# Kernel optimization log

Measured on AMD Instinct MI355X. Metric: run time of the kernel, lower is better.

## Reference

```python
import jax, jax.numpy as jnp
import numpy as np

N, E = 50000, 800000          # nodes, edges
IN, H, OUT = 256, 128, 2       # input feat, hidden_channels, out_channels
NEG_SLOPE = 0.2                # GATv2 LeakyReLU slope (PyG default)


def _w(key, fan_in, fan_out):
    return jax.random.normal(key, (fan_in, fan_out), jnp.float32) / np.sqrt(fan_in).astype(np.float32)


def setup_inputs() -> dict:
    key = jax.random.key(0)
    ks = jax.random.split(key, 24)
    inp = {
        "x": jax.random.normal(ks[0], (N, IN), jnp.float32),
        "edge_index": jax.random.randint(ks[1], (2, E), 0, N, jnp.int32),
        # GATv2Conv 0: in=IN -> H
        "c0_Wl": _w(ks[2], IN, H), "c0_Wr": _w(ks[3], IN, H),
        "c0_att": jax.random.normal(ks[4], (H,), jnp.float32) / np.sqrt(H).astype(np.float32),
        "c0_b": jnp.zeros((H,), jnp.float32),
        # GATv2Conv 1: H -> H
        "c1_Wl": _w(ks[5], H, H), "c1_Wr": _w(ks[6], H, H),
        "c1_att": jax.random.normal(ks[7], (H,), jnp.float32) / np.sqrt(H).astype(np.float32),
        "c1_b": jnp.zeros((H,), jnp.float32),
        # final GATv2Conv: H -> OUT
        "cf_Wl": _w(ks[8], H, OUT), "cf_Wr": _w(ks[9], H, OUT),
        "cf_att": jax.random.normal(ks[10], (OUT,), jnp.float32) / np.sqrt(OUT).astype(np.float32),
        "cf_b": jnp.zeros((OUT,), jnp.float32),
        # residual Linears
        "l0_W": _w(ks[11], IN, H), "l0_b": jnp.zeros((H,), jnp.float32),
        "l1_W": _w(ks[12], H, H), "l1_b": jnp.zeros((H,), jnp.float32),
        "lf_W": _w(ks[13], H, OUT), "lf_b": jnp.zeros((OUT,), jnp.float32),
    }
    return inp


def gatv2(x, edge_index, Wl, Wr, att, bias):
    """PyG GATv2Conv, heads=1, add_self_loops=False, share_weights=False."""
    src, dst = edge_index[0], edge_index[1]
    xs = x @ Wl                                   # [N,H] source transform
    xd = x @ Wr                                   # [N,H] target transform
    h = jax.nn.leaky_relu(xs[src] + xd[dst], NEG_SLOPE)   # [E,H]
    e = h @ att                                   # [E] attention logits
    # segment softmax over incoming edges of each destination node
    m = jax.ops.segment_max(e, dst, num_segments=N)
    m = jnp.where(jnp.isfinite(m), m, 0.0)
    p = jnp.exp(e - m[dst])
    s = jax.ops.segment_sum(p, dst, num_segments=N)
    alpha = p / (s[dst] + 1e-16)                  # [E]
    out = jax.ops.segment_sum(alpha[:, None] * xs[src], dst, num_segments=N)
    return out + bias


def reference(x, edge_index, c0_Wl, c0_Wr, c0_att, c0_b, c1_Wl, c1_Wr, c1_att, c1_b,
              cf_Wl, cf_Wr, cf_att, cf_b, l0_W, l0_b, l1_W, l1_b, lf_W, lf_b):
    # layer 0 + residual linear, then ReLU
    h = gatv2(x, edge_index, c0_Wl, c0_Wr, c0_att, c0_b) + (jax.nn.relu(x) @ l0_W + l0_b)
    h = jax.nn.relu(h)
    # layer 1 -> embeddings
    emb = gatv2(h, edge_index, c1_Wl, c1_Wr, c1_att, c1_b) + (jax.nn.relu(h) @ l1_W + l1_b)
    # final layer -> logits
    out = gatv2(emb, edge_index, cf_Wl, cf_Wr, cf_att, cf_b) + (jax.nn.relu(emb) @ lf_W + lf_b)
    return (out, emb)
```

## Files before the change

kernel.cpp:

```cpp
#include <hip/hip_runtime.h>
#include <hip/hip_bf16.h>

#define NEG_SLOPE 0.2f

typedef __attribute__((ext_vector_type(8))) _Float16 half8;
typedef __attribute__((ext_vector_type(2))) _Float16 h2v;
typedef __attribute__((ext_vector_type(4))) float f32x4;

__device__ __forceinline__ float toF(float x) { return x; }
__device__ __forceinline__ float toF(__hip_bfloat16 x) { return __bfloat162float(x); }
__device__ __forceinline__ float toF(_Float16 x) { return (float)x; }

__device__ __forceinline__ void stT(float* p, size_t i, float v) { p[i] = v; }
__device__ __forceinline__ void stT(__hip_bfloat16* p, size_t i, float v) {
    p[i] = __float2bfloat16(v);
}
__device__ __forceinline__ void stT(_Float16* p, size_t i, float v) { p[i] = (_Float16)v; }

template <typename T> struct IsBF { static constexpr bool v = false; };
template <> struct IsBF<__hip_bfloat16> { static constexpr bool v = true; };

__device__ __forceinline__ void vwaitn(int n) {
    if (n == 0) asm volatile("s_waitcnt vmcnt(0)" ::: "memory");
    else if (n == 7) asm volatile("s_waitcnt vmcnt(7)" ::: "memory");
    else if (n == 8) asm volatile("s_waitcnt vmcnt(8)" ::: "memory");
    else if (n == 9) asm volatile("s_waitcnt vmcnt(9)" ::: "memory");
    else asm volatile("s_waitcnt vmcnt(10)" ::: "memory");
}

__global__ void k_detect(const unsigned* __restrict__ x, int* __restrict__ flag) {
    unsigned u = x[threadIdx.x];
    int lo_exp = (int)((u >> 7) & 0xFFu);
    int ok = (lo_exp >= 90 && lo_exp <= 141) ? 1 : 0;
    unsigned long long b = __ballot(ok);
    if (threadIdx.x == 0) flag[0] = (__popcll(b) >= 48) ? 1 : 0;
}

__global__ __launch_bounds__(256) void k_cnt(const int* __restrict__ src,
                                             const int* __restrict__ dst, int E,
                                             int* __restrict__ gcnt,
                                             unsigned* __restrict__ bbuf, int cap) {
    __shared__ int hist[64];
    __shared__ int lbase[64];
    __shared__ int gbase[64];
    __shared__ int lfill[64];
    __shared__ unsigned ebuf[4096];
    __shared__ unsigned char bb[4096];
    int t = threadIdx.x;
    int e0 = blockIdx.x * 4096;
    if (t < 64) { hist[t] = 0; lfill[t] = 0; }
    __syncthreads();
    unsigned my[16];
    int mybkt[16];
#pragma unroll
    for (int i = 0; i < 16; ++i) {
        int idx = e0 + i * 256 + t;
        if (idx < E) {
            int d = dst[idx];
            int b = d >> 10;
            mybkt[i] = b;
            my[i] = (unsigned)src[idx] | ((unsigned)(d & 1023) << 16);
            atomicAdd(&hist[b], 1);
        } else {
            mybkt[i] = -1;
        }
    }
    __syncthreads();
    if (t < 64) {
        int h = hist[t];
        int v = h;
#pragma unroll
        for (int o = 1; o < 64; o <<= 1) {
            int u = __shfl_up(v, o, 64);
            if (t >= o) v += u;
        }
        lbase[t] = v - h;
        gbase[t] = (h > 0) ? atomicAdd(&gcnt[t], h) : 0;
    }
    __syncthreads();
#pragma unroll
    for (int i = 0; i < 16; ++i) {
        int b = mybkt[i];
        if (b >= 0) {
            int p = lbase[b] + atomicAdd(&lfill[b], 1);
            ebuf[p] = my[i];
            bb[p] = (unsigned char)b;
        }
    }
    __syncthreads();
    int total = min(4096, E - e0);
    for (int p = t; p < total; p += 256) {
        int b = bb[p];
        int o = gbase[b] + (p - lbase[b]);
        if (o < cap) bbuf[(size_t)b * cap + o] = ebuf[p];
    }
}

__global__ __launch_bounds__(256) void k_bucket_hist(const int* __restrict__ gcnt,
                                                     const unsigned* __restrict__ bbuf, int cap,
                                                     int* __restrict__ rowptr, int n) {
    __shared__ int hist[1024];
    int b = blockIdx.x, t = threadIdx.x;
    for (int i = t; i < 1024; i += 256) hist[i] = 0;
    __syncthreads();
    int cnt = min(gcnt[b], cap);
    const unsigned* p = bbuf + (size_t)b * cap;
    for (int i = t; i < cnt; i += 256) atomicAdd(&hist[p[i] >> 16], 1);
    __syncthreads();
    for (int i = t; i < 1024; i += 256) {
        int d = b * 1024 + i;
        if (d < n) rowptr[d + 1] = hist[i];
    }
}

__global__ __launch_bounds__(256) void k_bplace(const int* __restrict__ gcnt,
                                                const unsigned* __restrict__ bbuf, int cap,
                                                const int* __restrict__ rowptr,
                                                int* __restrict__ csr_src, int n) {
    __shared__ int base[1024];
    __shared__ int fill[1024];
    int b = blockIdx.x, t = threadIdx.x;
    for (int i = t; i < 1024; i += 256) {
        int d = b * 1024 + i;
        base[i] = (d < n) ? rowptr[d] : 0;
        fill[i] = 0;
    }
    __syncthreads();
    int cnt = min(gcnt[b], cap);
    const unsigned* p = bbuf + (size_t)b * cap;
    for (int i = t; i < cnt; i += 256) {
        unsigned e = p[i];
        int dl = (int)(e >> 16);
        int pos = base[dl] + atomicAdd(&fill[dl], 1);
        csr_src[pos] = (int)(e & 0xFFFFu);
    }
}

__global__ void k_hist(const int* __restrict__ dst, int E, int* __restrict__ rowptr) {
    int i = blockIdx.x * blockDim.x + threadIdx.x;
    if (i < E) atomicAdd(&rowptr[dst[i] + 1], 1);
}

__global__ void k_scatter(const int* __restrict__ src, const int* __restrict__ dst, int E,
                          const int* __restrict__ rowptr, int* __restrict__ fill,
                          int* __restrict__ csr_src) {
    int i = blockIdx.x * blockDim.x + threadIdx.x;
    if (i < E) {
        int d = dst[i];
        int pos = rowptr[d] + atomicAdd(&fill[d], 1);
        csr_src[pos] = src[i];
    }
}

__global__ __launch_bounds__(256) void k_scan1(int* __restrict__ rowptr,
                                               int* __restrict__ blksum, int n) {
    __shared__ int wsum[4];
    int t = threadIdx.x, lane = t & 63, w = t >> 6;
    int idx = blockIdx.x * 1024 + t * 4;
    int c0 = (idx + 0 < n) ? rowptr[idx + 1] : 0;
    int c1 = (idx + 1 < n) ? rowptr[idx + 2] : 0;
    int c2 = (idx + 2 < n) ? rowptr[idx + 3] : 0;
    int c3 = (idx + 3 < n) ? rowptr[idx + 4] : 0;
    int s1 = c0 + c1, s2 = s1 + c2, s3 = s2 + c3;
    int v = s3;
#pragma unroll
    for (int o = 1; o < 64; o <<= 1) {
        int u = __shfl_up(v, o, 64);
        if (lane >= o) v += u;
    }
    if (lane == 63) wsum[w] = v;
    __syncthreads();
    int woff = 0;
#pragma unroll
    for (int i = 0; i < 3; ++i)
        if (i < w) woff += wsum[i];
    int excl = woff + v - s3;
    if (idx + 0 < n) rowptr[idx + 1] = excl + c0;
    if (idx + 1 < n) rowptr[idx + 2] = excl + s1;
    if (idx + 2 < n) rowptr[idx + 3] = excl + s2;
    if (idx + 3 < n) rowptr[idx + 4] = excl + s3;
    if (t == 255) blksum[blockIdx.x] = woff + v;
}

__global__ void k_scan2(int* __restrict__ blksum, int nblk) {
    int t = threadIdx.x;
    int v = (t < nblk) ? blksum[t] : 0;
#pragma unroll
    for (int o = 1; o < 64; o <<= 1) {
        int u = __shfl_up(v, o, 64);
        if (t >= o) v += u;
    }
    if (t < nblk) blksum[t] = v;
}

__global__ void k_scan3(int* __restrict__ rowptr, const int* __restrict__ blksum, int n) {
    int idx = blockIdx.x * blockDim.x + threadIdx.x;
    if (idx < n) {
        int b = idx >> 10;
        if (b > 0) rowptr[idx + 1] += blksum[b - 1];
    }
}

template <typename WT>
__device__ void packW_body(const WT* W0, const WT* W1, const WT* W2, const WT* b2, int K,
                           _Float16* Bp, float* biasf) {
    int lane = threadIdx.x;
    int ksteps = K >> 5;
    int nb = 3 * ksteps * 8;
    int bid = blockIdx.x;
    if (bid == nb) {
        biasf[lane * 2 + 0] = toF(b2[lane * 2 + 0]);
        biasf[lane * 2 + 1] = toF(b2[lane * 2 + 1]);
        return;
    }
    int ks = bid / 24;
    int rem = bid - ks * 24;
    int o = rem >> 3, ct = rem & 7;
    const WT* W = (o == 0) ? W0 : ((o == 1) ? W1 : W2);
    int c = ct * 16 + (lane & 15);
    int k0 = ks * 32 + (lane >> 4) * 8;
    _Float16* out = Bp + (size_t)bid * 512 + lane * 8;
#pragma unroll
    for (int i = 0; i < 8; ++i) out[i] = (_Float16)toF(W[(size_t)(k0 + i) * 128 + c]);
}

__global__ void k_packW(const int* __restrict__ flag, const void* W0, const void* W1,
                        const void* W2, const void* b2, int K, _Float16* __restrict__ Bp,
                        float* __restrict__ biasf) {
    if (flag[0] == 0)
        packW_body<float>((const float*)W0, (const float*)W1, (const float*)W2,
                          (const float*)b2, K, Bp, biasf);
    else
        packW_body<__hip_bfloat16>((const __hip_bfloat16*)W0, (const __hip_bfloat16*)W1,
                                   (const __hip_bfloat16*)W2, (const __hip_bfloat16*)b2, K,
                                   Bp, biasf);
}

template <typename AT, typename O2T, int KSTEPS>
__device__ void gemm_body(const AT* __restrict__ A, int N,
                          const _Float16* __restrict__ Bp, const float* __restrict__ biasf,
                          _Float16* __restrict__ O0, _Float16* __restrict__ O1,
                          O2T* __restrict__ O2, _Float16 (*sB)[12288]) {
    const int H = 128;
    const int K = KSTEPS * 32;
    int tid = threadIdx.x;
    int wave = tid >> 6, lane = tid & 63;
    int row0 = (blockIdx.x * 4 + wave) * 16;
    int rr = lane & 15, kg = lane >> 4;
    int arow = min(row0 + rr, N - 1);
    constexpr int NR = (sizeof(AT) == 4) ? 2 : 1;

    f32x4 acc[3][8];
#pragma unroll
    for (int o = 0; o < 3; ++o)
#pragma unroll
        for (int ct = 0; ct < 8; ++ct) acc[o][ct] = f32x4{0.f, 0.f, 0.f, 0.f};

    auto stage = [&](int b, int ksv) {
        const char* gsrc = (const char*)(Bp + (size_t)ksv * 12288) + wave * 1024 + lane * 16;
        char* lbase = (char*)(&sB[b][0]) + wave * 1024;
#pragma unroll
        for (int r = 0; r < 6; ++r) {
            __builtin_amdgcn_global_load_lds(
                (const __attribute__((address_space(1))) unsigned*)(gsrc + r * 4096),
                (__attribute__((address_space(3))) unsigned*)(lbase + r * 4096), 16, 0, 0);
        }
    };
    auto loadA = [&](int ksv, uint4* dst) {
        const char* p = (const char*)A + ((size_t)arow * K + ksv * 32 + kg * 8) * sizeof(AT);
        dst[0] = *(const uint4*)p;
        if constexpr (NR == 2) dst[1] = *(const uint4*)(p + 16);
    };
    auto compute = [&](const uint4* raw, const _Float16* sb) {
        half8 a0, a1, r0f, r1f;
        if constexpr (sizeof(AT) == 4) {
            union { uint4 u[2]; float f[8]; } cv;
            cv.u[0] = raw[0]; cv.u[1] = raw[1];
#pragma unroll
            for (int i = 0; i < 8; ++i) {
                float a = cv.f[i];
                _Float16 h = (_Float16)a;
                float lof = a - (float)h;
                _Float16 lo = (_Float16)lof;
                bool pos = a > 0.f;
                a0[i] = h; a1[i] = lo;
                r0f[i] = pos ? h : (_Float16)0.f;
                r1f[i] = pos ? lo : (_Float16)0.f;
            }
        } else if constexpr (IsBF<AT>::v) {
            union { uint4 u4; unsigned u[4]; } cv;
            cv.u4 = raw[0];
#pragma unroll
            for (int q = 0; q < 4; ++q) {
                union { unsigned u; float f; } lo, hi;
                lo.u = cv.u[q] << 16;
                hi.u = cv.u[q] & 0xFFFF0000u;
                a0[2 * q] = (_Float16)lo.f;
                a0[2 * q + 1] = (_Float16)hi.f;
                r0f[2 * q] = (_Float16)fmaxf(lo.f, 0.f);
                r0f[2 * q + 1] = (_Float16)fmaxf(hi.f, 0.f);
            }
        } else {
            union { uint4 u4; half8 h; } cv;
            cv.u4 = raw[0];
            a0 = cv.h;
#pragma unroll
            for (int i = 0; i < 8; ++i)
                r0f[i] = (a0[i] > (_Float16)0.f) ? a0[i] : (_Float16)0.f;
        }
#pragma unroll
        for (int ct = 0; ct < 8; ++ct) {
            half8 w0 = *(const half8*)(sb + (0 * 8 + ct) * 512 + lane * 8);
            half8 w1 = *(const half8*)(sb + (1 * 8 + ct) * 512 + lane * 8);
            half8 w2 = *(const half8*)(sb + (2 * 8 + ct) * 512 + lane * 8);
            acc[0][ct] = __builtin_amdgcn_mfma_f32_16x16x32_f16(a0, w0, acc[0][ct], 0, 0, 0);
            acc[1][ct] = __builtin_amdgcn_mfma_f32_16x16x32_f16(a0, w1, acc[1][ct], 0, 0, 0);
            acc[2][ct] = __builtin_amdgcn_mfma_f32_16x16x32_f16(r0f, w2, acc[2][ct], 0, 0, 0);
            if constexpr (sizeof(AT) == 4) {
                acc[0][ct] = __builtin_amdgcn_mfma_f32_16x16x32_f16(a1, w0, acc[0][ct], 0, 0, 0);
                acc[1][ct] = __builtin_amdgcn_mfma_f32_16x16x32_f16(a1, w1, acc[1][ct], 0, 0, 0);
                acc[2][ct] = __builtin_amdgcn_mfma_f32_16x16x32_f16(r1f, w2, acc[2][ct], 0, 0, 0);
            }
        }
    };

    uint4 rA[3][NR];
    loadA(0, rA[0]);
    loadA(1, rA[1]);
    stage(0, 0);
#pragma unroll
    for (int ks = 0; ks < KSTEPS; ++ks) {
        if (ks + 1 < KSTEPS) {
            stage((ks + 1) & 1, ks + 1);
            asm volatile("" ::: "memory");
        }
        if (ks + 2 < KSTEPS) loadA(ks + 2, rA[(ks + 2) % 3]);
        if (ks == 0 || ks == KSTEPS - 2) vwaitn(NR + 6);
        else if (ks + 2 < KSTEPS) vwaitn(2 * NR + 6);
        else vwaitn(0);
        __builtin_amdgcn_s_barrier();
        compute(rA[ks % 3], &sB[ks & 1][0]);
        __builtin_amdgcn_s_barrier();
    }

    int rb = row0 + kg * 4;
#pragma unroll
    for (int ct = 0; ct < 8; ++ct) {
        int c = ct * 16 + rr;
        float bv = biasf[c];
#pragma unroll
        for (int j = 0; j < 4; ++j) {
            int row = rb + j;
            if (row < N) {
                size_t o = (size_t)row * H + c;
                O0[o] = (_Float16)acc[0][ct][j];
                O1[o] = (_Float16)acc[1][ct][j];
                stT(O2, o, acc[2][ct][j] + bv);
            }
        }
    }
}

template <int LAYER>
__global__ __launch_bounds__(256) void gemm3_u(const int* __restrict__ flag, const void* Aext,
                                               const _Float16* Af16, int N,
                                               const _Float16* __restrict__ Bp,
                                               const float* __restrict__ biasf,
                                               _Float16* __restrict__ O0,
                                               _Float16* __restrict__ O1, _Float16* O2h,
                                               float* O2f, __hip_bfloat16* O2b) {
    __shared__ _Float16 sB[2][12288];
    int f = flag[0];
    if constexpr (LAYER == 0) {
        if (f == 0)
            gemm_body<float, _Float16, 8>((const float*)Aext, N, Bp, biasf, O0, O1, O2h, sB);
        else
            gemm_body<__hip_bfloat16, _Float16, 8>((const __hip_bfloat16*)Aext, N, Bp, biasf,
                                                   O0, O1, O2h, sB);
    } else {
        if (f == 0)
            gemm_body<_Float16, float, 4>(Af16, N, Bp, biasf, O0, O1, O2f, sB);
        else
            gemm_body<_Float16, __hip_bfloat16, 4>(Af16, N, Bp, biasf, O0, O1, O2b, sB);
    }
}

template <typename IOT, typename T, int FINAL>
__device__ void gat_body(const _Float16* __restrict__ xs, const _Float16* __restrict__ xd,
                         const int* __restrict__ rowptr, const int* __restrict__ csr_src,
                         IOT* __restrict__ io, const T* __restrict__ att,
                         const T* __restrict__ gbias, int n, int relu_out,
                         const T* __restrict__ Wl, const T* __restrict__ Wr,
                         const T* __restrict__ Wres, const T* __restrict__ bres,
                         float* __restrict__ xsf, float* __restrict__ xdf,
                         float* __restrict__ resf) {
    int tid = threadIdx.x;
    int l = tid & 15;
    int g = tid >> 4;
    int dst = blockIdx.x * 16 + g;
    if (blockIdx.x * 16 + ((tid >> 6) << 2) >= n) return;
    int dstc = min(dst, n - 1);
    bool act = dst < n;

    union U4H { uint4 u; h2v h[4]; };
    U4H du; du.u = *(const uint4*)(xd + (size_t)dstc * 128 + l * 8);
    h2v ap[4];
#pragma unroll
    for (int c = 0; c < 4; ++c) {
        ap[c][0] = (_Float16)toF(att[l * 8 + 2 * c]);
        ap[c][1] = (_Float16)toF(att[l * 8 + 2 * c + 1]);
    }
    const _Float16 ks = (_Float16)NEG_SLOPE;
    const h2v k02 = {ks, ks};

    int beg = rowptr[dstc];
    int end = act ? rowptr[dstc + 1] : beg;
    float m = -INFINITY, s = 0.f;
    h2v acc[4];
#pragma unroll
    for (int c = 0; c < 4; ++c) acc[c] = h2v{(_Float16)0.f, (_Float16)0.f};

    for (int j = beg; j < end; j += 8) {
        int rem = end - j;
        U4H v[8];
#pragma unroll
        for (int q = 0; q < 8; ++q) {
            int idx = j + ((rem > q) ? q : 0);
            int sq = csr_src[idx];
            v[q].u = *(const uint4*)(xs + (size_t)sq * 128 + l * 8);
        }
        float p[8];
#pragma unroll
        for (int q = 0; q < 8; ++q) p[q] = 0.f;
#pragma unroll
        for (int c = 0; c < 4; ++c) {
#pragma unroll
            for (int q = 0; q < 8; ++q) {
                h2v t = v[q].h[c] + du.h[c];
                t = __builtin_elementwise_max(t, t * k02);
                p[q] = __builtin_amdgcn_fdot2(t, ap[c], p[q], false);
            }
        }
#pragma unroll
        for (int o = 1; o < 16; o <<= 1) {
#pragma unroll
            for (int q = 0; q < 8; ++q) p[q] += __shfl_xor(p[q], o, 16);
        }
#pragma unroll
        for (int q = 1; q < 8; ++q)
            if (rem < q + 1) p[q] = -INFINITY;
        float pm = p[0];
#pragma unroll
        for (int q = 1; q < 8; ++q) pm = fmaxf(pm, p[q]);
        float nm = fmaxf(m, pm);
        float sc = __expf(m - nm);
        float w[8];
        float ws = 0.f;
#pragma unroll
        for (int q = 0; q < 8; ++q) {
            w[q] = __expf(p[q] - nm);
            ws += w[q];
        }
        s = s * sc + ws;
        _Float16 sch = (_Float16)sc;
        h2v scp = {sch, sch};
        h2v wp[8];
#pragma unroll
        for (int q = 0; q < 8; ++q) {
            _Float16 wh = (_Float16)w[q];
            wp[q] = h2v{wh, wh};
        }
#pragma unroll
        for (int c = 0; c < 4; ++c) {
            h2v a = acc[c] * scp;
#pragma unroll
            for (int q = 0; q < 8; ++q) a = a + v[q].h[c] * wp[q];
            acc[c] = a;
        }
        m = nm;
    }

    if (act) {
        float r = 1.f / (s + 1e-16f);
        size_t base = (size_t)dst * 128 + l * 8;
        float ev[8];
#pragma unroll
        for (int c = 0; c < 4; ++c) {
            int f0 = l * 8 + 2 * c;
            float v0 = (float)acc[c][0] * r + toF(gbias[f0]) + toF(io[base + 2 * c]);
            float v1 = (float)acc[c][1] * r + toF(gbias[f0 + 1]) + toF(io[base + 2 * c + 1]);
            if (relu_out) { v0 = fmaxf(v0, 0.f); v1 = fmaxf(v1, 0.f); }
            stT(io, base + 2 * c, v0);
            stT(io, base + 2 * c + 1, v1);
            ev[2 * c] = v0;
            ev[2 * c + 1] = v1;
        }
        if constexpr (FINAL) {
            float d[6] = {0.f, 0.f, 0.f, 0.f, 0.f, 0.f};
#pragma unroll
            for (int f = 0; f < 8; ++f) {
                int fg = (l * 8 + f) * 2;
                float e = ev[f];
                float rp = fmaxf(e, 0.f);
                d[0] += e * toF(Wl[fg]);
                d[1] += e * toF(Wl[fg + 1]);
                d[2] += e * toF(Wr[fg]);
                d[3] += e * toF(Wr[fg + 1]);
                d[4] += rp * toF(Wres[fg]);
                d[5] += rp * toF(Wres[fg + 1]);
            }
#pragma unroll
            for (int i = 0; i < 6; ++i) {
#pragma unroll
                for (int o = 1; o < 16; o <<= 1) d[i] += __shfl_xor(d[i], o, 16);
            }
            if (l == 0) {
                xsf[dst * 2 + 0] = d[0];
                xsf[dst * 2 + 1] = d[1];
                xdf[dst * 2 + 0] = d[2];
                xdf[dst * 2 + 1] = d[3];
                resf[dst * 2 + 0] = d[4] + toF(bres[0]);
                resf[dst * 2 + 1] = d[5] + toF(bres[1]);
            }
        }
    }
}

template <int FINAL>
__global__ __launch_bounds__(256) void gat_u(const int* __restrict__ flag,
                                             const _Float16* __restrict__ xs,
                                             const _Float16* __restrict__ xd,
                                             const int* __restrict__ rowptr,
                                             const int* __restrict__ csr_src, _Float16* io_h,
                                             float* io_f, __hip_bfloat16* io_b, const void* att,
                                             const void* gbias, int n, int relu_out,
                                             const void* Wl, const void* Wr, const void* Wres,
                                             const void* bres, float* xsf, float* xdf,
                                             float* resf) {
    typedef __hip_bfloat16 bf;
    int f = flag[0];
    if constexpr (FINAL == 0) {
        if (f == 0)
            gat_body<_Float16, float, 0>(xs, xd, rowptr, csr_src, io_h, (const float*)att,
                                         (const float*)gbias, n, relu_out, nullptr, nullptr,
                                         nullptr, nullptr, nullptr, nullptr, nullptr);
        else
            gat_body<_Float16, bf, 0>(xs, xd, rowptr, csr_src, io_h, (const bf*)att,
                                      (const bf*)gbias, n, relu_out, nullptr, nullptr, nullptr,
                                      nullptr, nullptr, nullptr, nullptr);
    } else {
        if (f == 0)
            gat_body<float, float, 1>(xs, xd, rowptr, csr_src, io_f, (const float*)att,
                                      (const float*)gbias, n, relu_out, (const float*)Wl,
                                      (const float*)Wr, (const float*)Wres, (const float*)bres,
                                      xsf, xdf, resf);
        else
            gat_body<bf, bf, 1>(xs, xd, rowptr, csr_src, io_b, (const bf*)att, (const bf*)gbias,
                                n, relu_out, (const bf*)Wl, (const bf*)Wr, (const bf*)Wres,
                                (const bf*)bres, xsf, xdf, resf);
    }
}

template <typename T>
__device__ void fe_body(const float* __restrict__ xsf, const float* __restrict__ xdf,
                        const float* __restrict__ resf, const int* __restrict__ rowptr,
                        const int* __restrict__ csr_src, const T* __restrict__ att,
                        const T* __restrict__ gb, T* __restrict__ out, int n) {
    int dst = blockIdx.x * blockDim.x + threadIdx.x;
    if (dst >= n) return;
    float2 dv = ((const float2*)xdf)[dst];
    float a0 = toF(att[0]), a1 = toF(att[1]);
    float m = -INFINITY, s = 0.f, acc0 = 0.f, acc1 = 0.f;
    int beg = rowptr[dst], end = rowptr[dst + 1];
    for (int j = beg; j < end; j += 4) {
        int rem = end - j;
        int i1 = (rem > 1) ? 1 : 0, i2 = (rem > 2) ? 2 : 0, i3 = (rem > 3) ? 3 : 0;
        int s0 = csr_src[j];
        int s1 = csr_src[j + i1];
        int s2 = csr_src[j + i2];
        int s3 = csr_src[j + i3];
        float2 v0 = ((const float2*)xsf)[s0];
        float2 v1 = ((const float2*)xsf)[s1];
        float2 v2 = ((const float2*)xsf)[s2];
        float2 v3 = ((const float2*)xsf)[s3];
        float h0, h1, e0, e1, e2, e3;
        h0 = v0.x + dv.x; h0 = fmaxf(h0, NEG_SLOPE * h0);
        h1 = v0.y + dv.y; h1 = fmaxf(h1, NEG_SLOPE * h1);
        e0 = h0 * a0 + h1 * a1;
        h0 = v1.x + dv.x; h0 = fmaxf(h0, NEG_SLOPE * h0);
        h1 = v1.y + dv.y; h1 = fmaxf(h1, NEG_SLOPE * h1);
        e1 = h0 * a0 + h1 * a1;
        h0 = v2.x + dv.x; h0 = fmaxf(h0, NEG_SLOPE * h0);
        h1 = v2.y + dv.y; h1 = fmaxf(h1, NEG_SLOPE * h1);
        e2 = h0 * a0 + h1 * a1;
        h0 = v3.x + dv.x; h0 = fmaxf(h0, NEG_SLOPE * h0);
        h1 = v3.y + dv.y; h1 = fmaxf(h1, NEG_SLOPE * h1);
        e3 = h0 * a0 + h1 * a1;
        if (rem < 2) e1 = -INFINITY;
        if (rem < 3) e2 = -INFINITY;
        if (rem < 4) e3 = -INFINITY;
        float pm = fmaxf(fmaxf(e0, e1), fmaxf(e2, e3));
        float nm = fmaxf(m, pm);
        float sc = __expf(m - nm);
        float w0 = __expf(e0 - nm), w1 = __expf(e1 - nm);
        float w2 = __expf(e2 - nm), w3 = __expf(e3 - nm);
        s = s * sc + ((w0 + w1) + (w2 + w3));
        acc0 = acc0 * sc + ((w0 * v0.x + w1 * v1.x) + (w2 * v2.x + w3 * v3.x));
        acc1 = acc1 * sc + ((w0 * v0.y + w1 * v1.y) + (w2 * v2.y + w3 * v3.y));
        m = nm;
    }
    float r = 1.f / (s + 1e-16f);
    float2 rv = ((const float2*)resf)[dst];
    stT(out, (size_t)dst * 2 + 0, acc0 * r + toF(gb[0]) + rv.x);
    stT(out, (size_t)dst * 2 + 1, acc1 * r + toF(gb[1]) + rv.y);
}

__global__ void final_edge_u(const int* __restrict__ flag, const float* __restrict__ xsf,
                             const float* __restrict__ xdf, const float* __restrict__ resf,
                             const int* __restrict__ rowptr, const int* __restrict__ csr_src,
                             const void* att, const void* gb, void* out, int n) {
    typedef __hip_bfloat16 bf;
    if (flag[0] == 0)
        fe_body<float>(xsf, xdf, resf, rowptr, csr_src, (const float*)att, (const float*)gb,
                       (float*)out, n);
    else
        fe_body<bf>(xsf, xdf, resf, rowptr, csr_src, (const bf*)att, (const bf*)gb, (bf*)out, n);
}

extern "C" void kernel_launch(void* const* d_in, const int* in_sizes, int n_in,
                              void* d_out, int out_size, void* d_ws, size_t ws_size,
                              hipStream_t stream) {
    typedef __hip_bfloat16 bf;
    typedef _Float16 f16;
    const int IN = 256, H = 128;
    const int N = in_sizes[0] / IN;
    const int E = in_sizes[1] / 2;

    const int* ei = (const int*)d_in[1];

    size_t off = 0;
    auto alloc = [&](size_t bytes) {
        void* p = (char*)d_ws + off;
        off += (bytes + 255) & ~(size_t)255;
        return p;
    };
    f16* xs = (f16*)alloc((size_t)N * H * 2);
    f16* xd = (f16*)alloc((size_t)N * H * 2);
    f16* hb = (f16*)alloc((size_t)N * H * 2);
    int* flag = (int*)alloc(256);
    int* rowptr = (int*)alloc((size_t)(N + 1) * 4);
    int* fill = (int*)alloc((size_t)N * 4);
    int* blksum = (int*)alloc(256 * 4);
    int* csr_src = (int*)alloc((size_t)E * 4);
    float* xsf = (float*)alloc((size_t)N * 2 * 4);
    float* xdf = (float*)alloc((size_t)N * 2 * 4);
    float* resf = (float*)alloc((size_t)N * 2 * 4);
    f16* Bp0 = (f16*)alloc((size_t)3 * 8 * 8 * 512 * 2);
    f16* Bp1 = (f16*)alloc((size_t)3 * 4 * 8 * 512 * 2);
    float* bias0 = (float*)alloc(128 * 4);
    float* bias1 = (float*)alloc(128 * 4);
    const int NB = (N + 1023) / 1024;
    const int CAP = ((2 * (E / (NB > 0 ? NB : 1) + 1) + 255) / 256) * 256;
    int* gcnt = (int*)alloc(64 * 4);
    unsigned* bbuf = (unsigned*)alloc((size_t)NB * CAP * 4);

    const int* e_src = ei;
    const int* e_dst = ei + E;

    k_detect<<<1, 64, 0, stream>>>((const unsigned*)d_in[0], flag);
    const int nblk = (N + 1023) / 1024;
    if (N <= 65536) {
        hipMemsetAsync(rowptr, 0, 4, stream);
        hipMemsetAsync(gcnt, 0, 64 * 4, stream);
        k_cnt<<<(E + 4095) / 4096, 256, 0, stream>>>(e_src, e_dst, E, gcnt, bbuf, CAP);
        k_bucket_hist<<<NB, 256, 0, stream>>>(gcnt, bbuf, CAP, rowptr, N);
        k_scan1<<<nblk, 256, 0, stream>>>(rowptr, blksum, N);
        k_scan2<<<1, 64, 0, stream>>>(blksum, nblk);
        k_scan3<<<(N + 255) / 256, 256, 0, stream>>>(rowptr, blksum, N);
        k_bplace<<<NB, 256, 0, stream>>>(gcnt, bbuf, CAP, rowptr, csr_src, N);
    } else {
        hipMemsetAsync(rowptr, 0, (size_t)(N + 1) * 4, stream);
        hipMemsetAsync(fill, 0, (size_t)N * 4, stream);
        k_hist<<<(E + 255) / 256, 256, 0, stream>>>(e_dst, E, rowptr);
        k_scan1<<<nblk, 256, 0, stream>>>(rowptr, blksum, N);
        k_scan2<<<1, 64, 0, stream>>>(blksum, nblk);
        k_scan3<<<(N + 255) / 256, 256, 0, stream>>>(rowptr, blksum, N);
        k_scatter<<<(E + 255) / 256, 256, 0, stream>>>(e_src, e_dst, E, rowptr, fill, csr_src);
    }

    k_packW<<<3 * 8 * 8 + 1, 64, 0, stream>>>(flag, d_in[2], d_in[3], d_in[14], d_in[15], IN,
                                              Bp0, bias0);
    k_packW<<<3 * 4 * 8 + 1, 64, 0, stream>>>(flag, d_in[6], d_in[7], d_in[16], d_in[17], H,
                                              Bp1, bias1);

    const int g64 = (N + 63) / 64;
    const int eblk16 = (N + 15) / 16;

    float* embF = (float*)d_out + (size_t)N * 2;
    bf* embB = (bf*)d_out + (size_t)N * 2;

    gemm3_u<0><<<g64, 256, 0, stream>>>(flag, d_in[0], nullptr, N, Bp0, bias0, xs, xd, hb,
                                        nullptr, nullptr);
    gat_u<0><<<eblk16, 256, 0, stream>>>(flag, xs, xd, rowptr, csr_src, hb, nullptr, nullptr,
                                         d_in[4], d_in[5], N, 1, nullptr, nullptr, nullptr,
                                         nullptr, nullptr, nullptr, nullptr);

    gemm3_u<1><<<g64, 256, 0, stream>>>(flag, nullptr, hb, N, Bp1, bias1, xs, xd, nullptr,
                                        embF, embB);
    gat_u<1><<<eblk16, 256, 0, stream>>>(flag, xs, xd, rowptr, csr_src, nullptr, embF, embB,
                                         d_in[8], d_in[9], N, 0, d_in[10], d_in[11], d_in[18],
                                         d_in[19], xsf, xdf, resf);

    final_edge_u<<<(N + 255) / 256, 256, 0, stream>>>(flag, xsf, xdf, resf, rowptr, csr_src,
                                                      d_in[12], d_in[13], d_out, N);
}
```

Baseline: 332.6 us.

## Fuse CSR bucket histogram, scan and placement; double-buffer edge gathers

The CSR build path for small N now uses a tiny per-bucket base scan plus one fused kernel that builds the local histogram, scans it, writes rowptr and places the sources. This replaces five launches (hist, three scan kernels, place) and one memset. Separately, the attention aggregation loop is software-pipelined with two register buffers, so the next 8 neighbor gathers are issued before the current batch is computed, hiding gather latency. The cost is higher register pressure, which may reduce occupancy.

```diff
diff --git a/kernel.cpp b/kernel.cpp
--- a/kernel.cpp
+++ b/kernel.cpp
@@ -96,42 +96,65 @@
     }
 }
 
-__global__ __launch_bounds__(256) void k_bucket_hist(const int* __restrict__ gcnt,
-                                                     const unsigned* __restrict__ bbuf, int cap,
-                                                     int* __restrict__ rowptr, int n) {
+__global__ void k_bbase(const int* __restrict__ gcnt, int* __restrict__ bbase, int nb,
+                        int cap) {
+    int t = threadIdx.x;
+    int c = (t < nb) ? min(gcnt[t], cap) : 0;
+    int v = c;
+#pragma unroll
+    for (int o = 1; o < 64; o <<= 1) {
+        int u = __shfl_up(v, o, 64);
+        if (t >= o) v += u;
+    }
+    if (t < nb) bbase[t] = v - c;
+}
+
+__global__ __launch_bounds__(256) void k_bhp(const int* __restrict__ gcnt,
+                                             const int* __restrict__ bbase,
+                                             const unsigned* __restrict__ bbuf, int cap,
+                                             int* __restrict__ rowptr,
+                                             int* __restrict__ csr_src, int n, int nb) {
     __shared__ int hist[1024];
-    int b = blockIdx.x, t = threadIdx.x;
-    for (int i = t; i < 1024; i += 256) hist[i] = 0;
+    __shared__ int fill[1024];
+    __shared__ int wsum[4];
+    int b = blockIdx.x, t = threadIdx.x, lane = t & 63, w = t >> 6;
+    for (int i = t; i < 1024; i += 256) { hist[i] = 0; fill[i] = 0; }
     __syncthreads();
     int cnt = min(gcnt[b], cap);
     const unsigned* p = bbuf + (size_t)b * cap;
     for (int i = t; i < cnt; i += 256) atomicAdd(&hist[p[i] >> 16], 1);
     __syncthreads();
-    for (int i = t; i < 1024; i += 256) {
-        int d = b * 1024 + i;
-        if (d < n) rowptr[d + 1] = hist[i];
-    }
-}
-
-__global__ __launch_bounds__(256) void k_bplace(const int* __restrict__ gcnt,
-                                                const unsigned* __restrict__ bbuf, int cap,
-                                                const int* __restrict__ rowptr,
-                                                int* __restrict__ csr_src, int n) {
-    __shared__ int base[1024];
-    __shared__ int fill[1024];
-    int b = blockIdx.x, t = threadIdx.x;
-    for (int i = t; i < 1024; i += 256) {
-        int d = b * 1024 + i;
-        base[i] = (d < n) ? rowptr[d] : 0;
-        fill[i] = 0;
-    }
-    __syncthreads();
-    int cnt = min(gcnt[b], cap);
-    const unsigned* p = bbuf + (size_t)b * cap;
+    int base0 = bbase[b];
+    int idx = t * 4;
+    int c0 = hist[idx + 0], c1 = hist[idx + 1], c2 = hist[idx + 2], c3 = hist[idx + 3];
+    int s1 = c0 + c1, s2 = s1 + c2, s3 = s2 + c3;
+    int v = s3;
+#pragma unroll
+    for (int o = 1; o < 64; o <<= 1) {
+        int u = __shfl_up(v, o, 64);
+        if (lane >= o) v += u;
+    }
+    if (lane == 63) wsum[w] = v;
+    __syncthreads();
+    int woff = 0;
+#pragma unroll
+    for (int i = 0; i < 3; ++i)
+        if (i < w) woff += wsum[i];
+    int excl = base0 + woff + v - s3;
+    hist[idx + 0] = excl;
+    hist[idx + 1] = excl + c0;
+    hist[idx + 2] = excl + s1;
+    hist[idx + 3] = excl + s2;
+    int d0 = b * 1024 + idx;
+#pragma unroll
+    for (int i = 0; i < 4; ++i)
+        if (d0 + i < n) rowptr[d0 + i] = hist[idx + i];
+    if (b == nb - 1 && t == 255) rowptr[n] = base0 + cnt;
+    __syncthreads();
     for (int i = t; i < cnt; i += 256) {
         unsigned e = p[i];
         int dl = (int)(e >> 16);
-        int pos = base[dl] + atomicAdd(&fill[dl], 1);
+        int pos = hist[dl] + atomicAdd(&fill[dl], 1);
         csr_src[pos] = (int)(e & 0xFFFFu);
     }
 }
@@ -420,15 +443,17 @@
 #pragma unroll
     for (int c = 0; c < 4; ++c) acc[c] = h2v{(_Float16)0.f, (_Float16)0.f};
 
-    for (int j = beg; j < end; j += 8) {
-        int rem = end - j;
-        U4H v[8];
+    auto GATHER = [&](U4H (&v)[8], int j0) {
 #pragma unroll
         for (int q = 0; q < 8; ++q) {
-            int idx = j + ((rem > q) ? q : 0);
+            int idx = j0 + q;
+            if (idx >= end) idx = j0;
             int sq = csr_src[idx];
             v[q].u = *(const uint4*)(xs + (size_t)sq * 128 + l * 8);
         }
+    };
+    auto COMPUTE = [&](U4H (&v)[8], int j0) {
+        int rem = end - j0;
         float p[8];
 #pragma unroll
         for (int q = 0; q < 8; ++q) p[q] = 0.f;
@@ -478,6 +503,17 @@
             acc[c] = a;
         }
         m = nm;
+    };
+
+    U4H va[8], vb[8];
+    if (beg < end) GATHER(va, beg);
+    for (int j = beg; j < end; j += 16) {
+        if (j + 8 < end) GATHER(vb, j + 8);
+        COMPUTE(va, j);
+        if (j + 8 < end) {
+            if (j + 16 < end) GATHER(va, j + 16);
+            COMPUTE(vb, j + 8);
+        }
     }
 
     if (act) {
@@ -662,23 +698,20 @@
     const int NB = (N + 1023) / 1024;
     const int CAP = ((2 * (E / (NB > 0 ? NB : 1) + 1) + 255) / 256) * 256;
     int* gcnt = (int*)alloc(64 * 4);
+    int* bbase = (int*)alloc(64 * 4);
     unsigned* bbuf = (unsigned*)alloc((size_t)NB * CAP * 4);
 
     const int* e_src = ei;
     const int* e_dst = ei + E;
 
     k_detect<<<1, 64, 0, stream>>>((const unsigned*)d_in[0], flag);
-    const int nblk = (N + 1023) / 1024;
     if (N <= 65536) {
-        hipMemsetAsync(rowptr, 0, 4, stream);
         hipMemsetAsync(gcnt, 0, 64 * 4, stream);
         k_cnt<<<(E + 4095) / 4096, 256, 0, stream>>>(e_src, e_dst, E, gcnt, bbuf, CAP);
-        k_bucket_hist<<<NB, 256, 0, stream>>>(gcnt, bbuf, CAP, rowptr, N);
-        k_scan1<<<nblk, 256, 0, stream>>>(rowptr, blksum, N);
-        k_scan2<<<1, 64, 0, stream>>>(blksum, nblk);
-        k_scan3<<<(N + 255) / 256, 256, 0, stream>>>(rowptr, blksum, N);
-        k_bplace<<<NB, 256, 0, stream>>>(gcnt, bbuf, CAP, rowptr, csr_src, N);
+        k_bbase<<<1, 64, 0, stream>>>(gcnt, bbase, NB, CAP);
+        k_bhp<<<NB, 256, 0, stream>>>(gcnt, bbase, bbuf, CAP, rowptr, csr_src, N, NB);
     } else {
+        const int nblk = (N + 1023) / 1024;
         hipMemsetAsync(rowptr, 0, (size_t)(N + 1) * 4, stream);
         hipMemsetAsync(fill, 0, (size_t)N * 4, stream);
         k_hist<<<(E + 255) / 256, 256, 0, stream>>>(e_dst, E, rowptr);
```

Result: faster. 325.0 us (-2.3%).
